# Kernel tuning notes

Measured on AMD Instinct MI355X. Metric: run time of the kernel, lower is better.

The kernel has to match this reference:

```python
import jax, jax.numpy as jnp
import numpy as np

NEG_SLOPE = 0.2

def setup_inputs() -> dict:
    key = jax.random.key(0)
    k1, k2, k3, k4, k5 = jax.random.split(key, 5)
    B, N, IN_DIM, H, D = 4, 2048, 256, 4, 64
    x = jax.random.normal(k1, (B, N, IN_DIM), dtype=jnp.float32)
    A_mask = jax.random.randint(k2, (N, N), 0, 2, dtype=jnp.int32)
    # xavier-like scaled params
    W = jax.random.normal(k3, (IN_DIM, H * D), dtype=jnp.float32) * (1.0 / np.sqrt(IN_DIM))
    a_src = jax.random.normal(k4, (H, D), dtype=jnp.float32) * (1.0 / np.sqrt(D))
    a_dst = jax.random.normal(k5, (H, D), dtype=jnp.float32) * (1.0 / np.sqrt(D))
    return {"x": x, "A_mask": A_mask, "W": W, "a_src": a_src, "a_dst": a_dst}

def reference(x, A_mask, W, a_src, a_dst):
    B, N, _ = x.shape
    H, D = a_src.shape
    # h: [B, N, H, D]
    h = (x @ W).reshape(B, N, H, D)
    # per-node attention scores: [B, N, H]
    src = jnp.einsum('bnhd,hd->bnh', h, a_src)
    dst = jnp.einsum('bnhd,hd->bnh', h, a_dst)
    # logits: [B, H, N, N] = src_i + dst_j, then leaky_relu
    logits = src.transpose(0, 2, 1)[:, :, :, None] + dst.transpose(0, 2, 1)[:, :, None, :]
    logits = jnp.where(logits >= 0, logits, NEG_SLOPE * logits)
    # mask (shared across batch and heads)
    logits = jnp.where(A_mask[None, None, :, :] == 0, -jnp.inf, logits)
    attn = jax.nn.softmax(logits, axis=-1)  # [B, H, N, N]
    # weighted sum over neighbors
    out = jnp.einsum('bhnm,bmhd->bnhd', attn, h).reshape(B, N, H * D)
    return jax.nn.elu(out)
```

## Files before the change

kernel.cpp:

```cpp
#include <hip/hip_runtime.h>

typedef float  f32x4 __attribute__((ext_vector_type(4)));
typedef short  s16x8 __attribute__((ext_vector_type(8)));

__device__ __forceinline__ unsigned short f2bf(float f){
    unsigned int u = __float_as_uint(f);
    u = u + 0x7FFFu + ((u >> 16) & 1u);
    return (unsigned short)(u >> 16);
}

__global__ void k_prep(const float* __restrict__ W, unsigned short* __restrict__ WT,
                       const int* __restrict__ mask, unsigned int* __restrict__ bitsT){
    int bid = blockIdx.x;
    if (bid < 2048){
        int i = bid;
        int wave = threadIdx.x >> 6, lane = threadIdx.x & 63;
        for (int c = wave; c < 32; c += 4){
            int v = mask[i*2048 + c*64 + lane];
            unsigned long long b = __ballot(v != 0);
            if (lane == 0){
                bitsT[(2*c    )*2048 + i] = (unsigned int)(b & 0xFFFFFFFFu);
                bitsT[(2*c + 1)*2048 + i] = (unsigned int)(b >> 32);
            }
        }
    } else {
        int c = bid - 2048, k = threadIdx.x;
        WT[c*256 + k] = f2bf(W[k*256 + c]);
    }
}

__global__ __launch_bounds__(256) void k_gemm(const float* __restrict__ x,
        const unsigned short* __restrict__ WT,
        const float* __restrict__ a_src, const float* __restrict__ a_dst,
        unsigned short* __restrict__ hTt, float* __restrict__ E1a, float* __restrict__ E2a,
        float* __restrict__ F1a, float* __restrict__ F2a){
    const int wave = threadIdx.x >> 6, lane = threadIdx.x & 63;
    const int q = lane >> 4, t = lane & 15;
    const int m0 = blockIdx.x*64 + wave*16;
    const int head = blockIdx.y;
    f32x4 acc[4] = {{0,0,0,0},{0,0,0,0},{0,0,0,0},{0,0,0,0}};
    const int row = m0 + t;
    for (int k = 0; k < 256; k += 32){
        int kk = k + q*8;
        const float* xp = x + row*256 + kk;
        f32x4 x0 = *reinterpret_cast<const f32x4*>(xp);
        f32x4 x1 = *reinterpret_cast<const f32x4*>(xp + 4);
        s16x8 a;
#pragma unroll
        for (int j = 0; j < 4; j++){ a[j] = (short)f2bf(x0[j]); a[j+4] = (short)f2bf(x1[j]); }
#pragma unroll
        for (int dblk = 0; dblk < 4; dblk++){
            s16x8 bfr = *reinterpret_cast<const s16x8*>(WT + (head*64 + dblk*16 + t)*256 + kk);
            acc[dblk] = __builtin_amdgcn_mfma_f32_16x16x32_bf16(a, bfr, acc[dblk], 0, 0, 0);
        }
    }
    const int b = m0 >> 11;
    const int bh = b*4 + head;
    const int jb = (m0 & 2047) >> 4;
    float as_[4], ad_[4];
#pragma unroll
    for (int dblk = 0; dblk < 4; dblk++){
        as_[dblk] = a_src[head*64 + dblk*16 + t];
        ad_[dblk] = a_dst[head*64 + dblk*16 + t];
    }
#pragma unroll
    for (int reg = 0; reg < 4; reg++){
        float sv = acc[0][reg]*as_[0] + acc[1][reg]*as_[1] + acc[2][reg]*as_[2] + acc[3][reg]*as_[3];
        float dv = acc[0][reg]*ad_[0] + acc[1][reg]*ad_[1] + acc[2][reg]*ad_[2] + acc[3][reg]*ad_[3];
#pragma unroll
        for (int off = 1; off < 16; off <<= 1){
            sv += __shfl_xor(sv, off);
            dv += __shfl_xor(dv, off);
        }
        if (t == 0){
            int n = (m0 & 2047) + q*4 + reg;
            E1a[bh*2048 + n] = __expf(sv);
            E2a[bh*2048 + n] = __expf(0.2f*sv);
            F1a[bh*2048 + n] = __expf(dv);
            F2a[bh*2048 + n] = __expf(0.2f*dv);
        }
    }
#pragma unroll
    for (int dblk = 0; dblk < 4; dblk++){
        int d = dblk*16 + t;
#pragma unroll
        for (int reg = 0; reg < 4; reg++){
            int jj = q*4 + reg;
            hTt[((bh*128 + jb)*64 + d)*16 + jj] = f2bf(acc[dblk][reg]);
        }
    }
}

__device__ __forceinline__ s16x8 make_p2(unsigned int bs, float e1, float e2,
        f32x4 f1lo, f32x4 f1hi, f32x4 f2lo, f32x4 f2hi){
    float p[8];
#pragma unroll
    for (int jj = 0; jj < 8; jj++){
        float F1 = (jj < 4) ? f1lo[jj] : f1hi[jj-4];
        float F2 = (jj < 4) ? f2lo[jj] : f2hi[jj-4];
        float m1 = e1*F1, m2 = e2*F2;
        float pp = (m1 >= 1.0f) ? m1 : m2;
        p[jj] = ((bs >> jj) & 1u) ? pp : 0.0f;
    }
    union { unsigned int u[4]; s16x8 s; } pk;
#pragma unroll
    for (int z = 0; z < 4; z++)
        pk.u[z] = __builtin_amdgcn_perm(__float_as_uint(p[2*z+1]), __float_as_uint(p[2*z]), 0x07060302u);
    return pk.s;
}

__global__ __launch_bounds__(256, 4) void k_attn(const unsigned short* __restrict__ hTt,
        const unsigned int* __restrict__ bitsT, const float* __restrict__ E1a,
        const float* __restrict__ E2a, const float* __restrict__ F1a,
        const float* __restrict__ F2a, float* __restrict__ out){
    __shared__ float accL[4][16][64];
    __shared__ float Sl[4][16];
    const int bh = blockIdx.x;
    const int b = bh >> 2, head = bh & 3;
    const int wave = threadIdx.x >> 6, lane = threadIdx.x & 63;
    const int q = lane >> 4, t = lane & 15, q8 = q*8;
    const int i0 = blockIdx.y*32;
    const float E10 = E1a[bh*2048 + i0 + t];
    const float E20 = E2a[bh*2048 + i0 + t];
    const float E11 = E1a[bh*2048 + i0 + 16 + t];
    const float E21 = E2a[bh*2048 + i0 + 16 + t];
    const unsigned int* bT = bitsT + (wave*16)*2048 + i0 + t;
    const float* F1p = F1a + bh*2048 + wave*512 + q8;
    const float* F2p = F2a + bh*2048 + wave*512 + q8;
    const unsigned short* vB = hTt + bh*131072 + wave*32768 + (q>>1)*1024 + (q&1)*8 + t*16;
    f32x4 a00={0,0,0,0},a01={0,0,0,0},a02={0,0,0,0},a03={0,0,0,0};
    f32x4 a10={0,0,0,0},a11={0,0,0,0},a12={0,0,0,0},a13={0,0,0,0};
    f32x4 s0acc={0,0,0,0}, s1acc={0,0,0,0};
    s16x8 ones;
#pragma unroll
    for (int j = 0; j < 8; j++) ones[j] = (short)0x3F80;
    for (int it = 0; it < 16; ++it){
        const unsigned short* vp = vB + it*2048;
        s16x8 h0 = *reinterpret_cast<const s16x8*>(vp);
        s16x8 h1 = *reinterpret_cast<const s16x8*>(vp + 256);
        s16x8 h2 = *reinterpret_cast<const s16x8*>(vp + 512);
        s16x8 h3 = *reinterpret_cast<const s16x8*>(vp + 768);
        f32x4 f1lo = *reinterpret_cast<const f32x4*>(F1p + it*32);
        f32x4 f1hi = *reinterpret_cast<const f32x4*>(F1p + it*32 + 4);
        f32x4 f2lo = *reinterpret_cast<const f32x4*>(F2p + it*32);
        f32x4 f2hi = *reinterpret_cast<const f32x4*>(F2p + it*32 + 4);
        unsigned int bs0 = bT[it*2048]      >> q8;
        unsigned int bs1 = bT[it*2048 + 16] >> q8;
        s16x8 p0 = make_p2(bs0, E10, E20, f1lo, f1hi, f2lo, f2hi);
        s16x8 p1 = make_p2(bs1, E11, E21, f1lo, f1hi, f2lo, f2hi);
        a00 = __builtin_amdgcn_mfma_f32_16x16x32_bf16(p0, h0, a00, 0,0,0);
        a01 = __builtin_amdgcn_mfma_f32_16x16x32_bf16(p0, h1, a01, 0,0,0);
        a02 = __builtin_amdgcn_mfma_f32_16x16x32_bf16(p0, h2, a02, 0,0,0);
        a03 = __builtin_amdgcn_mfma_f32_16x16x32_bf16(p0, h3, a03, 0,0,0);
        s0acc = __builtin_amdgcn_mfma_f32_16x16x32_bf16(p0, ones, s0acc, 0,0,0);
        a10 = __builtin_amdgcn_mfma_f32_16x16x32_bf16(p1, h0, a10, 0,0,0);
        a11 = __builtin_amdgcn_mfma_f32_16x16x32_bf16(p1, h1, a11, 0,0,0);
        a12 = __builtin_amdgcn_mfma_f32_16x16x32_bf16(p1, h2, a12, 0,0,0);
        a13 = __builtin_amdgcn_mfma_f32_16x16x32_bf16(p1, h3, a13, 0,0,0);
        s1acc = __builtin_amdgcn_mfma_f32_16x16x32_bf16(p1, ones, s1acc, 0,0,0);
    }
#pragma unroll
    for (int half = 0; half < 2; half++){
        f32x4 c0 = half ? a10 : a00;
        f32x4 c1 = half ? a11 : a01;
        f32x4 c2 = half ? a12 : a02;
        f32x4 c3 = half ? a13 : a03;
        f32x4 sc = half ? s1acc : s0acc;
        if (half) __syncthreads();
#pragma unroll
        for (int reg = 0; reg < 4; reg++){
            int r = q*4 + reg;
            accL[wave][r][ 0 + t] = c0[reg];
            accL[wave][r][16 + t] = c1[reg];
            accL[wave][r][32 + t] = c2[reg];
            accL[wave][r][48 + t] = c3[reg];
        }
        if (t == 0){
#pragma unroll
            for (int reg = 0; reg < 4; reg++) Sl[wave][q*4 + reg] = sc[reg];
        }
        __syncthreads();
        const int tid = threadIdx.x;
        const int row = tid >> 4;
        const int d   = (tid & 15) * 4;
        f32x4 v0 = *reinterpret_cast<const f32x4*>(&accL[0][row][d]);
        f32x4 v1 = *reinterpret_cast<const f32x4*>(&accL[1][row][d]);
        f32x4 v2 = *reinterpret_cast<const f32x4*>(&accL[2][row][d]);
        f32x4 v3 = *reinterpret_cast<const f32x4*>(&accL[3][row][d]);
        float Ssum = Sl[0][row] + Sl[1][row] + Sl[2][row] + Sl[3][row];
        float rS = 1.0f / Ssum;
        f32x4 v;
#pragma unroll
        for (int c = 0; c < 4; c++){
            float vv = (v0[c] + v1[c] + v2[c] + v3[c]) * rS;
            v[c] = vv > 0.f ? vv : (__expf(vv) - 1.0f);
        }
        *reinterpret_cast<f32x4*>(out + (b*2048 + i0 + half*16 + row)*256 + head*64 + d) = v;
    }
}

extern "C" void kernel_launch(void* const* d_in, const int* in_sizes, int n_in,
                              void* d_out, int out_size, void* d_ws, size_t ws_size,
                              hipStream_t stream) {
    const float* x     = (const float*)d_in[0];
    const int*   Amask = (const int*)d_in[1];
    const float* W     = (const float*)d_in[2];
    const float* a_src = (const float*)d_in[3];
    const float* a_dst = (const float*)d_in[4];
    float* out = (float*)d_out;

    char* ws = (char*)d_ws;
    unsigned short* hTt   = (unsigned short*)(ws);
    unsigned int*   bitsT = (unsigned int*)(ws + (4u<<20));
    unsigned short* WT    = (unsigned short*)(ws + (4u<<20) + (512u<<10));
    float*          E1a   = (float*)(ws + (4u<<20) + (640u<<10));
    float*          E2a   = (float*)(ws + (4u<<20) + (768u<<10));
    float*          F1a   = (float*)(ws + (4u<<20) + (896u<<10));
    float*          F2a   = (float*)(ws + (4u<<20) + (1024u<<10));

    hipLaunchKernelGGL(k_prep, dim3(2304),    dim3(256), 0, stream, W, WT, Amask, bitsT);
    hipLaunchKernelGGL(k_gemm, dim3(128, 4),  dim3(256), 0, stream, x, WT, a_src, a_dst, hTt, E1a, E2a, F1a, F2a);
    hipLaunchKernelGGL(k_attn, dim3(16, 64),  dim3(256), 0, stream, hTt, bitsT, E1a, E2a, F1a, F2a, out);
}
```

Baseline: 112.8 us.

## Double attention row tile per block and store W in fragment-major layout

The attention kernel now processes 64 query rows per block instead of 32, using four accumulator sets. Each loaded h fragment and F1/F2 vector is reused across twice as many rows, which halves the number of blocks and the redundant V loads. Launch bounds drop to 3 waves per SIMD to allow the extra registers, which lowers occupancy. W is also pre-swizzled into a fragment-contiguous bf16 layout so that GEMM B-operand loads become contiguous.

```diff
diff --git a/kernel.cpp b/kernel.cpp
--- a/kernel.cpp
+++ b/kernel.cpp
@@ -9,7 +9,7 @@
     return (unsigned short)(u >> 16);
 }
 
-__global__ void k_prep(const float* __restrict__ W, unsigned short* __restrict__ WT,
+__global__ void k_prep(const float* __restrict__ W, unsigned short* __restrict__ WTf,
                        const int* __restrict__ mask, unsigned int* __restrict__ bitsT){
     int bid = blockIdx.x;
     if (bid < 2048){
@@ -24,13 +24,14 @@
             }
         }
     } else {
-        int c = bid - 2048, k = threadIdx.x;
-        WT[c*256 + k] = f2bf(W[k*256 + c]);
+        int dg = bid - 2048, k = threadIdx.x;
+        int dgT = dg >> 4, tt = dg & 15, kT = k >> 5, kj = k & 31;
+        WTf[((dgT*8 + kT)*16 + tt)*32 + kj] = f2bf(W[k*256 + dg]);
     }
 }
 
 __global__ __launch_bounds__(256) void k_gemm(const float* __restrict__ x,
-        const unsigned short* __restrict__ WT,
+        const unsigned short* __restrict__ WTf,
         const float* __restrict__ a_src, const float* __restrict__ a_dst,
         unsigned short* __restrict__ hTt, float* __restrict__ E1a, float* __restrict__ E2a,
         float* __restrict__ F1a, float* __restrict__ F2a){
@@ -50,7 +51,8 @@
         for (int j = 0; j < 4; j++){ a[j] = (short)f2bf(x0[j]); a[j+4] = (short)f2bf(x1[j]); }
 #pragma unroll
         for (int dblk = 0; dblk < 4; dblk++){
-            s16x8 bfr = *reinterpret_cast<const s16x8*>(WT + (head*64 + dblk*16 + t)*256 + kk);
+            s16x8 bfr = *reinterpret_cast<const s16x8*>(
+                WTf + (((head*4 + dblk)*8 + (k >> 5))*16 + t)*32 + q*8);
             acc[dblk] = __builtin_amdgcn_mfma_f32_16x16x32_bf16(a, bfr, acc[dblk], 0, 0, 0);
         }
     }
@@ -109,7 +111,7 @@
     return pk.s;
 }
 
-__global__ __launch_bounds__(256, 4) void k_attn(const unsigned short* __restrict__ hTt,
+__global__ __launch_bounds__(256, 3) void k_attn(const unsigned short* __restrict__ hTt,
         const unsigned int* __restrict__ bitsT, const float* __restrict__ E1a,
         const float* __restrict__ E2a, const float* __restrict__ F1a,
         const float* __restrict__ F2a, float* __restrict__ out){
@@ -119,18 +121,19 @@
     const int b = bh >> 2, head = bh & 3;
     const int wave = threadIdx.x >> 6, lane = threadIdx.x & 63;
     const int q = lane >> 4, t = lane & 15, q8 = q*8;
-    const int i0 = blockIdx.y*32;
-    const float E10 = E1a[bh*2048 + i0 + t];
-    const float E20 = E2a[bh*2048 + i0 + t];
-    const float E11 = E1a[bh*2048 + i0 + 16 + t];
-    const float E21 = E2a[bh*2048 + i0 + 16 + t];
+    const int i0 = blockIdx.y*64;
+    const float E10 = E1a[bh*2048 + i0 +  0 + t], E20 = E2a[bh*2048 + i0 +  0 + t];
+    const float E11 = E1a[bh*2048 + i0 + 16 + t], E21 = E2a[bh*2048 + i0 + 16 + t];
+    const float E12 = E1a[bh*2048 + i0 + 32 + t], E22 = E2a[bh*2048 + i0 + 32 + t];
+    const float E13 = E1a[bh*2048 + i0 + 48 + t], E23 = E2a[bh*2048 + i0 + 48 + t];
     const unsigned int* bT = bitsT + (wave*16)*2048 + i0 + t;
     const float* F1p = F1a + bh*2048 + wave*512 + q8;
     const float* F2p = F2a + bh*2048 + wave*512 + q8;
     const unsigned short* vB = hTt + bh*131072 + wave*32768 + (q>>1)*1024 + (q&1)*8 + t*16;
-    f32x4 a00={0,0,0,0},a01={0,0,0,0},a02={0,0,0,0},a03={0,0,0,0};
-    f32x4 a10={0,0,0,0},a11={0,0,0,0},a12={0,0,0,0},a13={0,0,0,0};
-    f32x4 s0acc={0,0,0,0}, s1acc={0,0,0,0};
+    f32x4 a00={0,0,0,0},a01={0,0,0,0},a02={0,0,0,0},a03={0,0,0,0},s0acc={0,0,0,0};
+    f32x4 a10={0,0,0,0},a11={0,0,0,0},a12={0,0,0,0},a13={0,0,0,0},s1acc={0,0,0,0};
+    f32x4 a20={0,0,0,0},a21={0,0,0,0},a22={0,0,0,0},a23={0,0,0,0},s2acc={0,0,0,0};
+    f32x4 a30={0,0,0,0},a31={0,0,0,0},a32={0,0,0,0},a33={0,0,0,0},s3acc={0,0,0,0};
     s16x8 ones;
 #pragma unroll
     for (int j = 0; j < 8; j++) ones[j] = (short)0x3F80;
@@ -144,29 +147,37 @@
         f32x4 f1hi = *reinterpret_cast<const f32x4*>(F1p + it*32 + 4);
         f32x4 f2lo = *reinterpret_cast<const f32x4*>(F2p + it*32);
         f32x4 f2hi = *reinterpret_cast<const f32x4*>(F2p + it*32 + 4);
-        unsigned int bs0 = bT[it*2048]      >> q8;
+        unsigned int bs0 = bT[it*2048 +  0] >> q8;
         unsigned int bs1 = bT[it*2048 + 16] >> q8;
+        unsigned int bs2 = bT[it*2048 + 32] >> q8;
+        unsigned int bs3 = bT[it*2048 + 48] >> q8;
         s16x8 p0 = make_p2(bs0, E10, E20, f1lo, f1hi, f2lo, f2hi);
-        s16x8 p1 = make_p2(bs1, E11, E21, f1lo, f1hi, f2lo, f2hi);
         a00 = __builtin_amdgcn_mfma_f32_16x16x32_bf16(p0, h0, a00, 0,0,0);
         a01 = __builtin_amdgcn_mfma_f32_16x16x32_bf16(p0, h1, a01, 0,0,0);
         a02 = __builtin_amdgcn_mfma_f32_16x16x32_bf16(p0, h2, a02, 0,0,0);
         a03 = __builtin_amdgcn_mfma_f32_16x16x32_bf16(p0, h3, a03, 0,0,0);
         s0acc = __builtin_amdgcn_mfma_f32_16x16x32_bf16(p0, ones, s0acc, 0,0,0);
+        s16x8 p1 = make_p2(bs1, E11, E21, f1lo, f1hi, f2lo, f2hi);
         a10 = __builtin_amdgcn_mfma_f32_16x16x32_bf16(p1, h0, a10, 0,0,0);
         a11 = __builtin_amdgcn_mfma_f32_16x16x32_bf16(p1, h1, a11, 0,0,0);
         a12 = __builtin_amdgcn_mfma_f32_16x16x32_bf16(p1, h2, a12, 0,0,0);
         a13 = __builtin_amdgcn_mfma_f32_16x16x32_bf16(p1, h3, a13, 0,0,0);
         s1acc = __builtin_amdgcn_mfma_f32_16x16x32_bf16(p1, ones, s1acc, 0,0,0);
-    }
-#pragma unroll
-    for (int half = 0; half < 2; half++){
-        f32x4 c0 = half ? a10 : a00;
-        f32x4 c1 = half ? a11 : a01;
-        f32x4 c2 = half ? a12 : a02;
-        f32x4 c3 = half ? a13 : a03;
-        f32x4 sc = half ? s1acc : s0acc;
-        if (half) __syncthreads();
+        s16x8 p2 = make_p2(bs2, E12, E22, f1lo, f1hi, f2lo, f2hi);
+        a20 = __builtin_amdgcn_mfma_f32_16x16x32_bf16(p2, h0, a20, 0,0,0);
+        a21 = __builtin_amdgcn_mfma_f32_16x16x32_bf16(p2, h1, a21, 0,0,0);
+        a22 = __builtin_amdgcn_mfma_f32_16x16x32_bf16(p2, h2, a22, 0,0,0);
+        a23 = __builtin_amdgcn_mfma_f32_16x16x32_bf16(p2, h3, a23, 0,0,0);
+        s2acc = __builtin_amdgcn_mfma_f32_16x16x32_bf16(p2, ones, s2acc, 0,0,0);
+        s16x8 p3 = make_p2(bs3, E13, E23, f1lo, f1hi, f2lo, f2hi);
+        a30 = __builtin_amdgcn_mfma_f32_16x16x32_bf16(p3, h0, a30, 0,0,0);
+        a31 = __builtin_amdgcn_mfma_f32_16x16x32_bf16(p3, h1, a31, 0,0,0);
+        a32 = __builtin_amdgcn_mfma_f32_16x16x32_bf16(p3, h2, a32, 0,0,0);
+        a33 = __builtin_amdgcn_mfma_f32_16x16x32_bf16(p3, h3, a33, 0,0,0);
+        s3acc = __builtin_amdgcn_mfma_f32_16x16x32_bf16(p3, ones, s3acc, 0,0,0);
+    }
+    auto epi = [&](f32x4 c0, f32x4 c1, f32x4 c2, f32x4 c3, f32x4 sc, int fi){
+        if (fi) __syncthreads();
 #pragma unroll
         for (int reg = 0; reg < 4; reg++){
             int r = q*4 + reg;
@@ -195,8 +206,12 @@
             float vv = (v0[c] + v1[c] + v2[c] + v3[c]) * rS;
             v[c] = vv > 0.f ? vv : (__expf(vv) - 1.0f);
         }
-        *reinterpret_cast<f32x4*>(out + (b*2048 + i0 + half*16 + row)*256 + head*64 + d) = v;
-    }
+        *reinterpret_cast<f32x4*>(out + (b*2048 + i0 + fi*16 + row)*256 + head*64 + d) = v;
+    };
+    epi(a00, a01, a02, a03, s0acc, 0);
+    epi(a10, a11, a12, a13, s1acc, 1);
+    epi(a20, a21, a22, a23, s2acc, 2);
+    epi(a30, a31, a32, a33, s3acc, 3);
 }
 
 extern "C" void kernel_launch(void* const* d_in, const int* in_sizes, int n_in,
@@ -212,13 +227,13 @@
     char* ws = (char*)d_ws;
     unsigned short* hTt   = (unsigned short*)(ws);
     unsigned int*   bitsT = (unsigned int*)(ws + (4u<<20));
-    unsigned short* WT    = (unsigned short*)(ws + (4u<<20) + (512u<<10));
+    unsigned short* WTf   = (unsigned short*)(ws + (4u<<20) + (512u<<10));
     float*          E1a   = (float*)(ws + (4u<<20) + (640u<<10));
     float*          E2a   = (float*)(ws + (4u<<20) + (768u<<10));
     float*          F1a   = (float*)(ws + (4u<<20) + (896u<<10));
     float*          F2a   = (float*)(ws + (4u<<20) + (1024u<<10));
 
-    hipLaunchKernelGGL(k_prep, dim3(2304),    dim3(256), 0, stream, W, WT, Amask, bitsT);
-    hipLaunchKernelGGL(k_gemm, dim3(128, 4),  dim3(256), 0, stream, x, WT, a_src, a_dst, hTt, E1a, E2a, F1a, F2a);
-    hipLaunchKernelGGL(k_attn, dim3(16, 64),  dim3(256), 0, stream, hTt, bitsT, E1a, E2a, F1a, F2a, out);
-}
+    hipLaunchKernelGGL(k_prep, dim3(2304),    dim3(256), 0, stream, W, WTf, Amask, bitsT);
+    hipLaunchKernelGGL(k_gemm, dim3(128, 4),  dim3(256), 0, stream, x, WTf, a_src, a_dst, hTt, E1a, E2a, F1a, F2a);
+    hipLaunchKernelGGL(k_attn, dim3(16, 32),  dim3(256), 0, stream, hTt, bitsT, E1a, E2a, F1a, F2a, out);
+}
```

New measurement: 112.1 us. About the same (-0.7%).
